# Optimization experiments

Hardware: AMD Instinct MI355X
Metric: run time of the kernel (lower is better)

## Reference

```python
import jax, jax.numpy as jnp
import numpy as np

B, N, T, F_IN, F_OUT = 4, 2048, 12, 32, 32
ALPHA = 0.2  # leaky relu negative slope
NEG_INF = -9e15


def setup_inputs() -> dict:
    key = jax.random.key(0)
    k = jax.random.split(key, 6)
    x = jax.random.normal(k[0], (B, N, T, F_IN), dtype=jnp.float32)
    adj = jax.random.randint(k[1], (N, N), 0, 2, dtype=jnp.int32)
    W = jax.random.normal(k[2], (T * F_IN, T * F_OUT), dtype=jnp.float32) * 0.05
    a = jax.random.normal(k[3], (2 * T * F_OUT, 1), dtype=jnp.float32) * 0.05
    conv_w = jax.random.normal(k[4], (T, T, 3), dtype=jnp.float32) * 0.1  # (out_ch, in_ch, k)
    conv_b = jnp.zeros((T,), dtype=jnp.float32)
    return {"x": x, "adj": adj, "W": W, "a": a, "conv_w": conv_w, "conv_b": conv_b}


def reference(x, adj, W, a, conv_w, conv_b):
    Bz, Nn, Tt, Fi = x.shape
    Fo = W.shape[1] // Tt
    # temporal conv: channels = timesteps, length = nodes*features
    xt = x.transpose(0, 2, 1, 3).reshape(Bz, Tt, Nn * Fi)  # (B,T,L)
    xt = jax.lax.conv_general_dilated(
        xt, conv_w, window_strides=(1,), padding=[(1, 1)],
        dimension_numbers=("NCH", "OIH", "NCH")) + conv_b[None, :, None]
    xt = xt.reshape(Bz, Tt, Nn, Fi).transpose(0, 2, 1, 3).reshape(Bz, Nn, Tt * Fi)
    Wh = xt @ W  # (B, N, T*Fo)
    # e[b,i,j] = leakyrelu(Wh[b,i].a1 + Wh[b,j].a2)  -- avoids O(N^2 * 2F) concat
    a1 = a[: Tt * Fo, 0]
    a2 = a[Tt * Fo:, 0]
    f1 = Wh @ a1  # (B, N)
    f2 = Wh @ a2  # (B, N)
    e = jax.nn.leaky_relu(f1[:, :, None] + f2[:, None, :], negative_slope=ALPHA)
    e = jnp.where(adj[None, :, :] > 0, e, NEG_INF)
    attn = jax.nn.softmax(e, axis=-1)  # (B, N, N); dropout omitted (eval mode)
    h_prime = attn @ Wh  # (B, N, T*Fo)
    return jax.nn.elu(h_prime).reshape(Bz, Nn, Tt, Fo)
```

## Files before the change

### kernel.cpp

```cpp
#include <hip/hip_runtime.h>

using short8 = __attribute__((ext_vector_type(8))) short;
using f32x4  = __attribute__((ext_vector_type(4))) float;
using f32x16 = __attribute__((ext_vector_type(16))) float;

__device__ __forceinline__ unsigned short f2bf(float f) {
  unsigned u = __float_as_uint(f);
  u += 0x7fffu + ((u >> 16) & 1u);
  return (unsigned short)(u >> 16);
}

__global__ __launch_bounds__(256) void transpose_f2b_kernel(const float* __restrict__ in,
                                                            unsigned short* __restrict__ out,
                                                            int rows, int cols) {
  __shared__ float tile[32][33];
  const int r0 = blockIdx.x * 32, c0 = blockIdx.y * 32;
  const int li = threadIdx.x >> 5, ci = threadIdx.x & 31;
#pragma unroll
  for (int p = 0; p < 4; ++p) {
    int r = li + p * 8;
    tile[r][ci] = in[(size_t)(r0 + r) * cols + c0 + ci];
  }
  __syncthreads();
#pragma unroll
  for (int p = 0; p < 4; ++p) {
    int c = li + p * 8;
    out[(size_t)(c0 + c) * rows + r0 + ci] = f2bf(tile[ci][c]);
  }
}

__global__ __launch_bounds__(256) void adjmask_kernel(const int* __restrict__ adj,
                                                      unsigned* __restrict__ adjm) {
  const int wv = (blockIdx.x << 2) + (threadIdx.x >> 6);
  const int lane = threadIdx.x & 63;
  const int row = wv >> 5, j0 = (wv & 31) << 6;
  unsigned long long mask = __ballot(adj[(size_t)row * 2048 + j0 + lane] > 0);
  if (lane == 0) {
    adjm[row * 64 + (j0 >> 5)]     = (unsigned)mask;
    adjm[row * 64 + (j0 >> 5) + 1] = (unsigned)(mask >> 32);
  }
}

__global__ __launch_bounds__(512) void gemm_wh3_kernel(const float* __restrict__ x,
                                                       const float* __restrict__ cw,
                                                       const float* __restrict__ cb,
                                                       const unsigned short* __restrict__ Wt,
                                                       const float* __restrict__ a,
                                                       unsigned short* __restrict__ whp,
                                                       float* __restrict__ f1,
                                                       float* __restrict__ f2) {
  __shared__ __align__(16) char lds[49344 + 1792 + 256];
  float* xin = (float*)lds;
  unsigned short* atile = (unsigned short*)lds;
  unsigned short* wtile = (unsigned short*)(lds + 25088);
  float* cws = (float*)(lds + 49344);
  float* cbs = cws + 448;
  float* s1s = (float*)(lds + 49344 + 1792);
  float* s2s = s1s + 32;

  const int tid = threadIdx.x;
  const int rb = blockIdx.x;
  const int b = rb >> 6, jg = rb & 63;
  const int r0 = rb << 5;
  const int w = tid >> 6, lane = tid & 63;
  const int rg = w >> 2, cg = w & 3;
  const int il = lane & 15, kg = lane >> 4;

  if (tid < 432) cws[tid] = cw[tid];
  if (tid < 12) cbs[tid] = cb[tid];
  if (tid < 32) { s1s[tid] = 0.f; s2s[tid] = 0.f; }
  const float* xb = x + (size_t)b * 2048 * 12 * 32;
#pragma unroll
  for (int t = 0; t < 12; ++t) {
    for (int i = tid; i < 1026; i += 512) {
      const int gp = jg * 1024 + i - 1;
      float v = 0.f;
      if ((unsigned)gp < 65536u) v = xb[((size_t)(gp >> 5) * 12 + t) * 32 + (gp & 31)];
      xin[t * 1028 + i] = v;
    }
  }
  __syncthreads();

  const int ploc = tid * 2;
  float accv0[12], accv1[12];
#pragma unroll
  for (int to = 0; to < 12; ++to) { accv0[to] = cbs[to]; accv1[to] = cbs[to]; }
#pragma unroll
  for (int ti = 0; ti < 12; ++ti) {
    const float x0 = xin[ti * 1028 + ploc];
    const float x1 = xin[ti * 1028 + ploc + 1];
    const float x2 = xin[ti * 1028 + ploc + 2];
    const float x3 = xin[ti * 1028 + ploc + 3];
#pragma unroll
    for (int to = 0; to < 12; ++to) {
      const float* wp = &cws[(to * 12 + ti) * 3];
      const float w0 = wp[0], w1 = wp[1], w2 = wp[2];
      accv0[to] += x0 * w0 + x1 * w1 + x2 * w2;
      accv1[to] += x1 * w0 + x2 * w1 + x3 * w2;
    }
  }
  __syncthreads();

  {
    const int row = ploc >> 5, f = ploc & 31;
    unsigned* ap32 = (unsigned*)(atile + row * 392 + f);
#pragma unroll
    for (int to = 0; to < 12; ++to) {
      const unsigned lo = f2bf(accv0[to]), hi = f2bf(accv1[to]);
      ap32[to * 16] = lo | (hi << 16);
    }
  }
  __syncthreads();

  f32x4 acc[6];
#pragma unroll
  for (int t = 0; t < 6; ++t) acc[t] = (f32x4){0.f, 0.f, 0.f, 0.f};
  const unsigned short* arow = atile + (rg * 16 + il) * 392 + kg * 8;
#pragma unroll
  for (int kk = 0; kk < 12; ++kk) {
    short8 af = *reinterpret_cast<const short8*>(arow + kk * 32);
#pragma unroll
    for (int t = 0; t < 6; ++t) {
      const int c = cg * 96 + t * 16 + il;
      short8 bf = *reinterpret_cast<const short8*>(Wt + (size_t)c * 384 + kk * 32 + kg * 8);
      acc[t] = __builtin_amdgcn_mfma_f32_16x16x32_bf16(af, bf, acc[t], 0, 0, 0);
    }
  }
  float p1[4] = {0.f, 0.f, 0.f, 0.f}, p2[4] = {0.f, 0.f, 0.f, 0.f};
#pragma unroll
  for (int t = 0; t < 6; ++t) {
    const int c = cg * 96 + t * 16 + il;
    const float a1v = a[c], a2v = a[384 + c];
#pragma unroll
    for (int r = 0; r < 4; ++r) { p1[r] += acc[t][r] * a1v; p2[r] += acc[t][r] * a2v; }
  }
#pragma unroll
  for (int off = 1; off < 16; off <<= 1) {
#pragma unroll
    for (int r = 0; r < 4; ++r) { p1[r] += __shfl_xor(p1[r], off); p2[r] += __shfl_xor(p2[r], off); }
  }
  if (il == 0) {
#pragma unroll
    for (int r = 0; r < 4; ++r) {
      atomicAdd(&s1s[rg * 16 + kg * 4 + r], p1[r]);
      atomicAdd(&s2s[rg * 16 + kg * 4 + r], p2[r]);
    }
  }
#pragma unroll
  for (int t = 0; t < 6; ++t)
#pragma unroll
    for (int r = 0; r < 4; ++r)
      wtile[(rg * 16 + kg * 4 + r) * 392 + cg * 96 + t * 16 + il] = f2bf(acc[t][r]);
  __syncthreads();

#pragma unroll
  for (int rep = 0; rep < 3; ++rep) {
    const int flat = rep * 512 + tid;
    const int tile = flat >> 6, l = flat & 63;
    const int ct = tile >> 1, jh = tile & 1;
    const int l5 = l & 31, hw2 = l >> 5;
    short8 v;
#pragma unroll
    for (int e = 0; e < 8; ++e)
      v[e] = (short)wtile[(jh * 16 + hw2 * 8 + e) * 392 + ct * 32 + l5];
    *reinterpret_cast<short8*>((char*)whp +
        ((((size_t)b * 128 + jg * 2 + jh) * 12 + ct) << 10) + l * 16) = v;
  }
  if (tid < 32) { f1[r0 + tid] = s1s[tid]; f2[r0 + tid] = s2s[tid]; }
}

__global__ __launch_bounds__(256) void f2max_kernel(const float* __restrict__ f2,
                                                    float* __restrict__ gmax,
                                                    float* __restrict__ e2f2) {
  __shared__ float wm[4];
  const int b = blockIdx.x;
  const int tid = threadIdx.x;
  float m = -3.0e38f;
  for (int i = tid; i < 2048; i += 256) {
    const float v = f2[b * 2048 + i];
    m = fmaxf(m, v);
    float2 w; w.x = __expf(v); w.y = __expf(0.2f * v);
    *reinterpret_cast<float2*>(e2f2 + (size_t)(b * 2048 + i) * 2) = w;
  }
#pragma unroll
  for (int off = 32; off; off >>= 1) m = fmaxf(m, __shfl_xor(m, off));
  if ((tid & 63) == 0) wm[tid >> 6] = m;
  __syncthreads();
  if (tid == 0) gmax[b] = fmaxf(fmaxf(wm[0], wm[1]), fmaxf(wm[2], wm[3]));
}

__global__ __launch_bounds__(256, 2) void attn8_kernel(const float* __restrict__ f1,
                                                       const float* __restrict__ e2f2,
                                                       const unsigned* __restrict__ adjm,
                                                       const unsigned short* __restrict__ whp,
                                                       const float* __restrict__ gmax,
                                                       float* __restrict__ out) {
  __shared__ float red[4][32][96];
  __shared__ float dred[128];
  const int bi = blockIdx.x;
  const int ch = bi & 1;
  const int b  = (bi & 7) >> 1;
  const int i0 = (bi >> 3) << 5;
  const int tid = threadIdx.x;
  const int ks = tid >> 6;
  const int lane = tid & 63;
  const int l5 = lane & 31, hw = lane >> 5;
  const int hw8 = hw * 8;
  const int ig = i0 + l5;

  const uint4* ap_ = reinterpret_cast<const uint4*>(adjm + (size_t)ig * 64 + ks * 16);
  const uint4 aw0 = ap_[0], aw1 = ap_[1], aw2 = ap_[2], aw3 = ap_[3];

  const char* pA = (const char*)whp + ((((size_t)b * 128 + ks * 32) * 12) << 10) +
                   ch * 6144 + lane * 16;
  const char* pB = pA + 12288;
  const char* efbase = (const char*)e2f2 + (size_t)(b * 2048 + ks * 512 + hw8) * 8;

  const float f1v = f1[b * 2048 + ig];
  const float gm = gmax[b];
  const float mz = f1v + gm;
  const float m  = fmaxf(mz, 0.2f * mz);
  const float E1 = __expf(f1v - m);
  const float F1 = __expf(0.2f * f1v - m);
  const float T  = __expf(-f1v);

  const f32x16 zero16 = {0.f,0.f,0.f,0.f,0.f,0.f,0.f,0.f,0.f,0.f,0.f,0.f,0.f,0.f,0.f,0.f};
  f32x16 acc[6];
#pragma unroll
  for (int t = 0; t < 6; ++t) acc[t] = zero16;
  float denom = 0.f;

  short8 bA0, bA1, bA2, bA3, bA4, bA5, bB0, bB1, bB2, bB3, bB4, bB5;
  float4 efA0, efA1, efA2, efA3, efB0, efB1, efB2, efB3;

#define CAT3(X, Y, Z) X##Y##Z
#define EFV(S, N) CAT3(ef, S, N)
#define BFV(S, N) CAT3(b, S, N)

#define LOADB(S)                                                                        \
  { BFV(S,0) = *reinterpret_cast<const short8*>(p##S);                                  \
    BFV(S,1) = *reinterpret_cast<const short8*>(p##S + 1024);                           \
    BFV(S,2) = *reinterpret_cast<const short8*>(p##S + 2048);                           \
    BFV(S,3) = *reinterpret_cast<const short8*>(p##S + 3072);                           \
    const char* p4_ = p##S + 4096;                                                      \
    BFV(S,4) = *reinterpret_cast<const short8*>(p4_);                                   \
    BFV(S,5) = *reinterpret_cast<const short8*>(p4_ + 1024);                            \
    p##S += 24576; }

#define LOADEF(S, KK)                                                                   \
  { EFV(S,0) = *reinterpret_cast<const float4*>(efbase + (KK) * 128);                   \
    EFV(S,1) = *reinterpret_cast<const float4*>(efbase + (KK) * 128 + 16);              \
    EFV(S,2) = *reinterpret_cast<const float4*>(efbase + (KK) * 128 + 32);              \
    EFV(S,3) = *reinterpret_cast<const float4*>(efbase + (KK) * 128 + 48); }

#define PEL(EV, QV, BIT, DST)                                                           \
  { const bool pos_ = (EV) > T;                                                         \
    float jf_ = pos_ ? (EV) : (QV);                                                     \
    const float iv_ = pos_ ? E1 : F1;                                                   \
    jf_ = ((bits_ >> (BIT)) & 1u) ? jf_ : 0.f;                                          \
    DST = jf_ * iv_; }

#define PKBF(HI, LO) (((__float_as_uint(HI) + 0x8000u) & 0xffff0000u) |                 \
                      ((__float_as_uint(LO) + 0x8000u) >> 16))

#define STEP(S, W, SH, KK, DL)                                                          \
  { const unsigned bits_ = (W) >> ((SH) + hw8);                                         \
    float p0_, p1_, p2_, p3_, p4_, p5_, p6_, p7_;                                       \
    PEL(EFV(S,0).x, EFV(S,0).y, 0, p0_)  PEL(EFV(S,0).z, EFV(S,0).w, 1, p1_)            \
    PEL(EFV(S,1).x, EFV(S,1).y, 2, p2_)  PEL(EFV(S,1).z, EFV(S,1).w, 3, p3_)            \
    PEL(EFV(S,2).x, EFV(S,2).y, 4, p4_)  PEL(EFV(S,2).z, EFV(S,2).w, 5, p5_)            \
    PEL(EFV(S,3).x, EFV(S,3).y, 6, p6_)  PEL(EFV(S,3).z, EFV(S,3).w, 7, p7_)            \
    denom += (((p0_ + p1_) + (p2_ + p3_)) + ((p4_ + p5_) + (p6_ + p7_)));               \
    union { unsigned u[4]; short8 s8; } cc;                                             \
    cc.u[0] = PKBF(p1_, p0_); cc.u[1] = PKBF(p3_, p2_);                                 \
    cc.u[2] = PKBF(p5_, p4_); cc.u[3] = PKBF(p7_, p6_);                                 \
    acc[0] = __builtin_amdgcn_mfma_f32_32x32x16_bf16(cc.s8, BFV(S,0), acc[0], 0, 0, 0); \
    acc[1] = __builtin_amdgcn_mfma_f32_32x32x16_bf16(cc.s8, BFV(S,1), acc[1], 0, 0, 0); \
    acc[2] = __builtin_amdgcn_mfma_f32_32x32x16_bf16(cc.s8, BFV(S,2), acc[2], 0, 0, 0); \
    acc[3] = __builtin_amdgcn_mfma_f32_32x32x16_bf16(cc.s8, BFV(S,3), acc[3], 0, 0, 0); \
    acc[4] = __builtin_amdgcn_mfma_f32_32x32x16_bf16(cc.s8, BFV(S,4), acc[4], 0, 0, 0); \
    acc[5] = __builtin_amdgcn_mfma_f32_32x32x16_bf16(cc.s8, BFV(S,5), acc[5], 0, 0, 0); \
    if (DL) { LOADB(S) LOADEF(S, (KK) + 2) } }

#define GROUP(AW, K0)                                                                   \
  STEP(A, AW.x, 0, (K0) + 0, 1)  STEP(B, AW.x, 16, (K0) + 1, 1)                         \
  STEP(A, AW.y, 0, (K0) + 2, 1)  STEP(B, AW.y, 16, (K0) + 3, 1)                         \
  STEP(A, AW.z, 0, (K0) + 4, 1)  STEP(B, AW.z, 16, (K0) + 5, 1)                         \
  STEP(A, AW.w, 0, (K0) + 6, 1)  STEP(B, AW.w, 16, (K0) + 7, 1)

#define GROUPL(AW, K0)                                                                  \
  STEP(A, AW.x, 0, (K0) + 0, 1)  STEP(B, AW.x, 16, (K0) + 1, 1)                         \
  STEP(A, AW.y, 0, (K0) + 2, 1)  STEP(B, AW.y, 16, (K0) + 3, 1)                         \
  STEP(A, AW.z, 0, (K0) + 4, 1)  STEP(B, AW.z, 16, (K0) + 5, 1)                         \
  STEP(A, AW.w, 0, (K0) + 6, 0)  STEP(B, AW.w, 16, (K0) + 7, 0)

  LOADB(A) LOADB(B)
  LOADEF(A, 0) LOADEF(B, 1)

  GROUP(aw0, 0)
  GROUP(aw1, 8)
  GROUP(aw2, 16)
  GROUPL(aw3, 24)

#undef LOADB
#undef LOADEF
#undef PEL
#undef PKBF
#undef STEP
#undef GROUP
#undef GROUPL
#undef CAT3
#undef EFV
#undef BFV

  float dn = denom + __shfl_xor(denom, 32);
  if (hw == 0) dred[ks * 32 + l5] = dn;

#pragma unroll
  for (int r = 0; r < 2; ++r) {
#pragma unroll
    for (int t3 = 0; t3 < 3; ++t3) {
      const int t = r * 3 + t3;
#pragma unroll
      for (int q = 0; q < 16; ++q) {
        const int row = (q & 3) + 8 * (q >> 2) + 4 * hw;
        red[ks][row][t3 * 32 + l5] = acc[t][q];
      }
    }
    __syncthreads();
    const size_t ob = ((size_t)b * 2048 + i0) * 384 + ch * 192 + r * 96;
#pragma unroll
    for (int p = 0; p < 12; ++p) {
      const int idx = p * 256 + tid;
      const int row = idx / 96;
      const int c = idx - row * 96;
      float v = red[0][row][c] + red[1][row][c] + red[2][row][c] + red[3][row][c];
      const float d = dred[row] + dred[32 + row] + dred[64 + row] + dred[96 + row];
      v /= d;
      v = v > 0.f ? v : expm1f(v);
      out[ob + (size_t)row * 384 + c] = v;
    }
    __syncthreads();
  }
}

extern "C" void kernel_launch(void* const* d_in, const int* in_sizes, int n_in,
                              void* d_out, int out_size, void* d_ws, size_t ws_size,
                              hipStream_t stream) {
  const float* x  = (const float*)d_in[0];
  const int* adj  = (const int*)d_in[1];
  const float* W  = (const float*)d_in[2];
  const float* a  = (const float*)d_in[3];
  const float* cw = (const float*)d_in[4];
  const float* cb = (const float*)d_in[5];
  float* out = (float*)d_out;

  char* ws = (char*)d_ws;
  unsigned short* Wt  = (unsigned short*)ws; ws += (size_t)147456 * 2;
  unsigned short* whp = (unsigned short*)ws; ws += (size_t)3145728 * 2;
  float* f1           = (float*)ws;          ws += (size_t)8192 * 4;
  float* f2           = (float*)ws;          ws += (size_t)8192 * 4;
  unsigned* adjm      = (unsigned*)ws;       ws += (size_t)2048 * 64 * 4;
  float* gmax         = (float*)ws;          ws += 64;
  float* e2f2         = (float*)ws;          ws += (size_t)8192 * 2 * 4;

  transpose_f2b_kernel<<<dim3(12, 12), 256, 0, stream>>>(W, Wt, 384, 384);
  adjmask_kernel<<<dim3(16384), 256, 0, stream>>>(adj, adjm);
  gemm_wh3_kernel<<<dim3(256), 512, 0, stream>>>(x, cw, cb, Wt, a, whp, f1, f2);
  f2max_kernel<<<dim3(4), 256, 0, stream>>>(f2, gmax, e2f2);
  attn8_kernel<<<dim3(512), 256, 0, stream>>>(f1, e2f2, adjm, whp, gmax, out);
}
```

Before: 88.87 us.

## Restructure attention kernel to stage Wh chunks in LDS via async global_load_lds

The attention kernel is rewritten. The block no longer splits K across four waves and reduces them through shared memory. Instead each block covers all 384 output columns for 32 rows: Wh chunks are double-buffered into LDS with global_load_lds, the attention-probability tiles are generated cooperatively and written to LDS, and each wave computes a 96-column slice over the full K range. This is meant to remove the cross-wave reduction and the duplicate probability generation across column halves, and to overlap loads with MFMA. In exchange the grid halves to 256 blocks, each iteration needs a block barrier, and about 104KB of LDS per block limits occupancy to one block per CU.

```diff
diff --git a/kernel.cpp b/kernel.cpp
--- a/kernel.cpp
+++ b/kernel.cpp
@@ -3,6 +3,9 @@
 using short8 = __attribute__((ext_vector_type(8))) short;
 using f32x4  = __attribute__((ext_vector_type(4))) float;
 using f32x16 = __attribute__((ext_vector_type(16))) float;
+
+typedef const __attribute__((address_space(1))) void* as1cv;
+typedef __attribute__((address_space(3))) void* as3v;
 
 __device__ __forceinline__ unsigned short f2bf(float f) {
   unsigned u = __float_as_uint(f);
@@ -189,33 +192,31 @@
   if (tid == 0) gmax[b] = fmaxf(fmaxf(wm[0], wm[1]), fmaxf(wm[2], wm[3]));
 }
 
-__global__ __launch_bounds__(256, 2) void attn8_kernel(const float* __restrict__ f1,
-                                                       const float* __restrict__ e2f2,
-                                                       const unsigned* __restrict__ adjm,
-                                                       const unsigned short* __restrict__ whp,
-                                                       const float* __restrict__ gmax,
-                                                       float* __restrict__ out) {
-  __shared__ float red[4][32][96];
-  __shared__ float dred[128];
+#define BBYTES 49152
+__global__ __launch_bounds__(256) void attn9_kernel(const float* __restrict__ f1,
+                                                    const float* __restrict__ e2f2,
+                                                    const unsigned* __restrict__ adjm,
+                                                    const unsigned short* __restrict__ whp,
+                                                    const float* __restrict__ gmax,
+                                                    float* __restrict__ out) {
+  __shared__ __align__(16) char lds[2 * BBYTES + 2 * 4096 + 128];
+  char* pbase = lds + 2 * BBYTES;
+  float* dsum = (float*)(lds + 2 * BBYTES + 2 * 4096);
+
   const int bi = blockIdx.x;
-  const int ch = bi & 1;
   const int b  = (bi & 7) >> 1;
-  const int i0 = (bi >> 3) << 5;
+  const int i0 = (((bi >> 3) << 1) | (bi & 1)) << 5;
   const int tid = threadIdx.x;
-  const int ks = tid >> 6;
-  const int lane = tid & 63;
-  const int l5 = lane & 31, hw = lane >> 5;
-  const int hw8 = hw * 8;
-  const int ig = i0 + l5;
-
-  const uint4* ap_ = reinterpret_cast<const uint4*>(adjm + (size_t)ig * 64 + ks * 16);
-  const uint4 aw0 = ap_[0], aw1 = ap_[1], aw2 = ap_[2], aw3 = ap_[3];
-
-  const char* pA = (const char*)whp + ((((size_t)b * 128 + ks * 32) * 12) << 10) +
-                   ch * 6144 + lane * 16;
-  const char* pB = pA + 12288;
-  const char* efbase = (const char*)e2f2 + (size_t)(b * 2048 + ks * 512 + hw8) * 8;
-
+  const int wv = tid >> 6, lane = tid & 63;
+  const int l5 = lane & 31;
+
+  const int prow = tid & 31;
+  const int khalf = tid >> 5;
+  const int kf = khalf >> 1, hw2 = khalf & 1;
+  const int ig = i0 + prow;
+
+  const float* e2f2b = e2f2 + (size_t)b * 2048 * 2;
+  const unsigned* adjr = adjm + (size_t)ig * 64;
   const float f1v = f1[b * 2048 + ig];
   const float gm = gmax[b];
   const float mz = f1v + gm;
@@ -223,125 +224,126 @@
   const float E1 = __expf(f1v - m);
   const float F1 = __expf(0.2f * f1v - m);
   const float T  = __expf(-f1v);
+  float dloc = 0.f;
+
+  if (tid < 32) dsum[tid] = 0.f;
+
+  const char* whpb = (const char*)whp + (((size_t)b * 128 * 12) << 10);
+  char* pwaddr = pbase  + kf * 1024 + (hw2 * 32 + prow) * 16;
+
+#define STAGE(CUR, CHUNK)                                                               \
+  { const char* src_ = whpb + (size_t)(CHUNK) * BBYTES + tid * 16;                      \
+    char* dst_ = lds + (CUR) * BBYTES + tid * 16;                                       \
+    _Pragma("unroll")                                                                   \
+    for (int s_ = 0; s_ < 12; ++s_)                                                     \
+      __builtin_amdgcn_global_load_lds((as1cv)(const void*)(src_ + s_ * 4096),          \
+                                       (as3v)(void*)(dst_ + s_ * 4096), 16, 0, 0); }
+
+#define PGEN(CUR, CHUNK)                                                                \
+  { const int j0_ = (CHUNK) * 64 + khalf * 8;                                           \
+    const float4* ep_ = (const float4*)(e2f2b + (size_t)j0_ * 2);                       \
+    const float4 q0_ = ep_[0], q1_ = ep_[1], q2_ = ep_[2], q3_ = ep_[3];                \
+    const unsigned wrd_ = adjr[(CHUNK) * 2 + (khalf >> 2)];                             \
+    const unsigned bits_ = (wrd_ >> ((khalf & 3) * 8)) & 0xffu;                         \
+    float pv_[8];                                                                       \
+    pv_[0] = (q0_.x > T) ? q0_.x * E1 : q0_.y * F1;                                     \
+    pv_[1] = (q0_.z > T) ? q0_.z * E1 : q0_.w * F1;                                     \
+    pv_[2] = (q1_.x > T) ? q1_.x * E1 : q1_.y * F1;                                     \
+    pv_[3] = (q1_.z > T) ? q1_.z * E1 : q1_.w * F1;                                     \
+    pv_[4] = (q2_.x > T) ? q2_.x * E1 : q2_.y * F1;                                     \
+    pv_[5] = (q2_.z > T) ? q2_.z * E1 : q2_.w * F1;                                     \
+    pv_[6] = (q3_.x > T) ? q3_.x * E1 : q3_.y * F1;                                     \
+    pv_[7] = (q3_.z > T) ? q3_.z * E1 : q3_.w * F1;                                     \
+    unsigned pk_[8];                                                                    \
+    float ds_ = 0.f;                                                                    \
+    _Pragma("unroll")                                                                   \
+    for (int e_ = 0; e_ < 8; ++e_) {                                                    \
+      float v_ = ((bits_ >> e_) & 1u) ? pv_[e_] : 0.f;                                  \
+      unsigned r_ = (__float_as_uint(v_) + 0x8000u) & 0xffff0000u;                      \
+      ds_ += __uint_as_float(r_);                                                       \
+      pk_[e_] = r_;                                                                     \
+    }                                                                                   \
+    dloc += ds_;                                                                        \
+    uint4 blob_;                                                                        \
+    blob_.x = pk_[1] | (pk_[0] >> 16);                                                  \
+    blob_.y = pk_[3] | (pk_[2] >> 16);                                                  \
+    blob_.z = pk_[5] | (pk_[4] >> 16);                                                  \
+    blob_.w = pk_[7] | (pk_[6] >> 16);                                                  \
+    *(uint4*)(pwaddr + (CUR) * 4096) = blob_; }
 
   const f32x16 zero16 = {0.f,0.f,0.f,0.f,0.f,0.f,0.f,0.f,0.f,0.f,0.f,0.f,0.f,0.f,0.f,0.f};
-  f32x16 acc[6];
-#pragma unroll
-  for (int t = 0; t < 6; ++t) acc[t] = zero16;
-  float denom = 0.f;
-
-  short8 bA0, bA1, bA2, bA3, bA4, bA5, bB0, bB1, bB2, bB3, bB4, bB5;
-  float4 efA0, efA1, efA2, efA3, efB0, efB1, efB2, efB3;
-
-#define CAT3(X, Y, Z) X##Y##Z
-#define EFV(S, N) CAT3(ef, S, N)
-#define BFV(S, N) CAT3(b, S, N)
-
-#define LOADB(S)                                                                        \
-  { BFV(S,0) = *reinterpret_cast<const short8*>(p##S);                                  \
-    BFV(S,1) = *reinterpret_cast<const short8*>(p##S + 1024);                           \
-    BFV(S,2) = *reinterpret_cast<const short8*>(p##S + 2048);                           \
-    BFV(S,3) = *reinterpret_cast<const short8*>(p##S + 3072);                           \
-    const char* p4_ = p##S + 4096;                                                      \
-    BFV(S,4) = *reinterpret_cast<const short8*>(p4_);                                   \
-    BFV(S,5) = *reinterpret_cast<const short8*>(p4_ + 1024);                            \
-    p##S += 24576; }
-
-#define LOADEF(S, KK)                                                                   \
-  { EFV(S,0) = *reinterpret_cast<const float4*>(efbase + (KK) * 128);                   \
-    EFV(S,1) = *reinterpret_cast<const float4*>(efbase + (KK) * 128 + 16);              \
-    EFV(S,2) = *reinterpret_cast<const float4*>(efbase + (KK) * 128 + 32);              \
-    EFV(S,3) = *reinterpret_cast<const float4*>(efbase + (KK) * 128 + 48); }
-
-#define PEL(EV, QV, BIT, DST)                                                           \
-  { const bool pos_ = (EV) > T;                                                         \
-    float jf_ = pos_ ? (EV) : (QV);                                                     \
-    const float iv_ = pos_ ? E1 : F1;                                                   \
-    jf_ = ((bits_ >> (BIT)) & 1u) ? jf_ : 0.f;                                          \
-    DST = jf_ * iv_; }
-
-#define PKBF(HI, LO) (((__float_as_uint(HI) + 0x8000u) & 0xffff0000u) |                 \
-                      ((__float_as_uint(LO) + 0x8000u) >> 16))
-
-#define STEP(S, W, SH, KK, DL)                                                          \
-  { const unsigned bits_ = (W) >> ((SH) + hw8);                                         \
-    float p0_, p1_, p2_, p3_, p4_, p5_, p6_, p7_;                                       \
-    PEL(EFV(S,0).x, EFV(S,0).y, 0, p0_)  PEL(EFV(S,0).z, EFV(S,0).w, 1, p1_)            \
-    PEL(EFV(S,1).x, EFV(S,1).y, 2, p2_)  PEL(EFV(S,1).z, EFV(S,1).w, 3, p3_)            \
-    PEL(EFV(S,2).x, EFV(S,2).y, 4, p4_)  PEL(EFV(S,2).z, EFV(S,2).w, 5, p5_)            \
-    PEL(EFV(S,3).x, EFV(S,3).y, 6, p6_)  PEL(EFV(S,3).z, EFV(S,3).w, 7, p7_)            \
-    denom += (((p0_ + p1_) + (p2_ + p3_)) + ((p4_ + p5_) + (p6_ + p7_)));               \
-    union { unsigned u[4]; short8 s8; } cc;                                             \
-    cc.u[0] = PKBF(p1_, p0_); cc.u[1] = PKBF(p3_, p2_);                                 \
-    cc.u[2] = PKBF(p5_, p4_); cc.u[3] = PKBF(p7_, p6_);                                 \
-    acc[0] = __builtin_amdgcn_mfma_f32_32x32x16_bf16(cc.s8, BFV(S,0), acc[0], 0, 0, 0); \
-    acc[1] = __builtin_amdgcn_mfma_f32_32x32x16_bf16(cc.s8, BFV(S,1), acc[1], 0, 0, 0); \
-    acc[2] = __builtin_amdgcn_mfma_f32_32x32x16_bf16(cc.s8, BFV(S,2), acc[2], 0, 0, 0); \
-    acc[3] = __builtin_amdgcn_mfma_f32_32x32x16_bf16(cc.s8, BFV(S,3), acc[3], 0, 0, 0); \
-    acc[4] = __builtin_amdgcn_mfma_f32_32x32x16_bf16(cc.s8, BFV(S,4), acc[4], 0, 0, 0); \
-    acc[5] = __builtin_amdgcn_mfma_f32_32x32x16_bf16(cc.s8, BFV(S,5), acc[5], 0, 0, 0); \
-    if (DL) { LOADB(S) LOADEF(S, (KK) + 2) } }
-
-#define GROUP(AW, K0)                                                                   \
-  STEP(A, AW.x, 0, (K0) + 0, 1)  STEP(B, AW.x, 16, (K0) + 1, 1)                         \
-  STEP(A, AW.y, 0, (K0) + 2, 1)  STEP(B, AW.y, 16, (K0) + 3, 1)                         \
-  STEP(A, AW.z, 0, (K0) + 4, 1)  STEP(B, AW.z, 16, (K0) + 5, 1)                         \
-  STEP(A, AW.w, 0, (K0) + 6, 1)  STEP(B, AW.w, 16, (K0) + 7, 1)
-
-#define GROUPL(AW, K0)                                                                  \
-  STEP(A, AW.x, 0, (K0) + 0, 1)  STEP(B, AW.x, 16, (K0) + 1, 1)                         \
-  STEP(A, AW.y, 0, (K0) + 2, 1)  STEP(B, AW.y, 16, (K0) + 3, 1)                         \
-  STEP(A, AW.z, 0, (K0) + 4, 1)  STEP(B, AW.z, 16, (K0) + 5, 1)                         \
-  STEP(A, AW.w, 0, (K0) + 6, 0)  STEP(B, AW.w, 16, (K0) + 7, 0)
-
-  LOADB(A) LOADB(B)
-  LOADEF(A, 0) LOADEF(B, 1)
-
-  GROUP(aw0, 0)
-  GROUP(aw1, 8)
-  GROUP(aw2, 16)
-  GROUPL(aw3, 24)
-
-#undef LOADB
-#undef LOADEF
-#undef PEL
-#undef PKBF
-#undef STEP
-#undef GROUP
-#undef GROUPL
-#undef CAT3
-#undef EFV
-#undef BFV
-
-  float dn = denom + __shfl_xor(denom, 32);
-  if (hw == 0) dred[ks * 32 + l5] = dn;
-
-#pragma unroll
-  for (int r = 0; r < 2; ++r) {
-#pragma unroll
-    for (int t3 = 0; t3 < 3; ++t3) {
-      const int t = r * 3 + t3;
-#pragma unroll
-      for (int q = 0; q < 16; ++q) {
-        const int row = (q & 3) + 8 * (q >> 2) + 4 * hw;
-        red[ks][row][t3 * 32 + l5] = acc[t][q];
-      }
+  f32x16 acc0 = zero16, acc1 = zero16, acc2 = zero16;
+
+  STAGE(0, 0)
+  PGEN(0, 0)
+  __syncthreads();
+
+  int cur = 0;
+  for (int t = 0; t < 32; ++t) {
+    if (t < 31) {
+      STAGE(cur ^ 1, t + 1)
+      PGEN(cur ^ 1, t + 1)
+    }
+    const char* bb = lds + cur * BBYTES;
+    const char* pb = pbase + cur * 4096;
+    short8 af0 = *(const short8*)(pb + lane * 16);
+    short8 af1 = *(const short8*)(pb + 1024 + lane * 16);
+    short8 af2 = *(const short8*)(pb + 2048 + lane * 16);
+    short8 af3 = *(const short8*)(pb + 3072 + lane * 16);
+    const char* bw = bb + (wv * 3) * 1024 + lane * 16;
+    {
+      short8 bf0 = *(const short8*)(bw);
+      short8 bf1 = *(const short8*)(bw + 12288);
+      short8 bf2 = *(const short8*)(bw + 24576);
+      short8 bf3 = *(const short8*)(bw + 36864);
+      acc0 = __builtin_amdgcn_mfma_f32_32x32x16_bf16(af0, bf0, acc0, 0, 0, 0);
+      acc0 = __builtin_amdgcn_mfma_f32_32x32x16_bf16(af1, bf1, acc0, 0, 0, 0);
+      acc0 = __builtin_amdgcn_mfma_f32_32x32x16_bf16(af2, bf2, acc0, 0, 0, 0);
+      acc0 = __builtin_amdgcn_mfma_f32_32x32x16_bf16(af3, bf3, acc0, 0, 0, 0);
+    }
+    {
+      short8 bf0 = *(const short8*)(bw + 1024);
+      short8 bf1 = *(const short8*)(bw + 12288 + 1024);
+      short8 bf2 = *(const short8*)(bw + 24576 + 1024);
+      short8 bf3 = *(const short8*)(bw + 36864 + 1024);
+      acc1 = __builtin_amdgcn_mfma_f32_32x32x16_bf16(af0, bf0, acc1, 0, 0, 0);
+      acc1 = __builtin_amdgcn_mfma_f32_32x32x16_bf16(af1, bf1, acc1, 0, 0, 0);
+      acc1 = __builtin_amdgcn_mfma_f32_32x32x16_bf16(af2, bf2, acc1, 0, 0, 0);
+      acc1 = __builtin_amdgcn_mfma_f32_32x32x16_bf16(af3, bf3, acc1, 0, 0, 0);
+    }
+    {
+      short8 bf0 = *(const short8*)(bw + 2048);
+      short8 bf1 = *(const short8*)(bw + 12288 + 2048);
+      short8 bf2 = *(const short8*)(bw + 24576 + 2048);
+      short8 bf3 = *(const short8*)(bw + 36864 + 2048);
+      acc2 = __builtin_amdgcn_mfma_f32_32x32x16_bf16(af0, bf0, acc2, 0, 0, 0);
+      acc2 = __builtin_amdgcn_mfma_f32_32x32x16_bf16(af1, bf1, acc2, 0, 0, 0);
+      acc2 = __builtin_amdgcn_mfma_f32_32x32x16_bf16(af2, bf2, acc2, 0, 0, 0);
+      acc2 = __builtin_amdgcn_mfma_f32_32x32x16_bf16(af3, bf3, acc2, 0, 0, 0);
     }
     __syncthreads();
-    const size_t ob = ((size_t)b * 2048 + i0) * 384 + ch * 192 + r * 96;
-#pragma unroll
-    for (int p = 0; p < 12; ++p) {
-      const int idx = p * 256 + tid;
-      const int row = idx / 96;
-      const int c = idx - row * 96;
-      float v = red[0][row][c] + red[1][row][c] + red[2][row][c] + red[3][row][c];
-      const float d = dred[row] + dred[32 + row] + dred[64 + row] + dred[96 + row];
-      v /= d;
-      v = v > 0.f ? v : expm1f(v);
-      out[ob + (size_t)row * 384 + c] = v;
-    }
-    __syncthreads();
-  }
+    cur ^= 1;
+  }
+#undef STAGE
+#undef PGEN
+
+  atomicAdd(&dsum[prow], dloc);
+  __syncthreads();
+
+  const int hw = lane >> 5;
+  const size_t ob = ((size_t)b * 2048 + i0) * 384 + wv * 96;
+#define OUTACC(ACCV, CT3)                                                               \
+  _Pragma("unroll")                                                                     \
+  for (int q = 0; q < 16; ++q) {                                                        \
+    const int row = (q & 3) + 8 * (q >> 2) + 4 * hw;                                    \
+    float v = ACCV[q] / dsum[row];                                                      \
+    v = v > 0.f ? v : expm1f(v);                                                        \
+    out[ob + (size_t)row * 384 + (CT3) * 32 + l5] = v;                                  \
+  }
+  OUTACC(acc0, 0)
+  OUTACC(acc1, 1)
+  OUTACC(acc2, 2)
+#undef OUTACC
 }
 
 extern "C" void kernel_launch(void* const* d_in, const int* in_sizes, int n_in,
@@ -368,5 +370,5 @@
   adjmask_kernel<<<dim3(16384), 256, 0, stream>>>(adj, adjm);
   gemm_wh3_kernel<<<dim3(256), 512, 0, stream>>>(x, cw, cb, Wt, a, whp, f1, f2);
   f2max_kernel<<<dim3(4), 256, 0, stream>>>(f2, gmax, e2f2);
-  attn8_kernel<<<dim3(512), 256, 0, stream>>>(f1, e2f2, adjm, whp, gmax, out);
-}
+  attn9_kernel<<<dim3(256), 256, 0, stream>>>(f1, e2f2, adjm, whp, gmax, out);
+}
```

New measurement: 113.3 us. +27.5%, slower.
